# Kernel optimization log

Measured on AMD Instinct MI355X. Metric: run time of the kernel, lower is better.

Reference implementation:

```python
import jax, jax.numpy as jnp
import numpy as np

FULL_ROW, FULL_COL = 512, 1024   # input_size
ROW, COL = 64, 128               # input_size / ratio 8
N_SAMPLE = ROW * COL             # 8192 sampled pixels
NUM_CLASSES = 19
C = 512                          # feature dim hardcoded in source


def setup_inputs() -> dict:
    key = jax.random.key(0)
    k1, k2, k3 = jax.random.split(key, 3)
    features_tensor = jax.random.normal(k1, (1, C, FULL_ROW, FULL_COL), jnp.float32)
    outputs = jax.random.normal(k2, (1, NUM_CLASSES, FULL_ROW, FULL_COL), jnp.float32)
    classes_prototypes = jax.random.normal(k3, (1, NUM_CLASSES, C), jnp.float32)
    # random.sample -> unique sorted indices into the full h*w grid
    idx = np.sort(np.random.default_rng(0).choice(FULL_ROW * FULL_COL, N_SAMPLE, replace=False))
    sample_index = jnp.asarray(idx, dtype=jnp.int32)
    return {
        "features_tensor": features_tensor,
        "outputs": outputs,
        "classes_prototypes": classes_prototypes,
        "sample_index": sample_index,
    }


def reference(features_tensor, outputs, classes_prototypes, sample_index):
    hw = FULL_ROW * FULL_COL
    # gather sampled pixel features: (1,C,H,W) -> (H*W, C) -> (N_SAMPLE, C)
    feats = features_tensor.transpose(0, 2, 3, 1).reshape(hw, C)[sample_index]
    # predicted class per sampled pixel (softmax over classes preserves argmax)
    class_ids = jnp.argmax(outputs[0], axis=0).reshape(hw)[sample_index]  # (N_SAMPLE,)
    protos = classes_prototypes[0]  # (NUM_CLASSES, C)
    # squared euclidean distance, clamped (disparity_mode 'E', dim==3 path)
    d = (jnp.sum(feats * feats, axis=-1, keepdims=True)
         - 2.0 * feats @ protos.T
         + jnp.sum(protos * protos, axis=-1))            # (N_SAMPLE, NUM_CLASSES)
    d = jnp.clip(d, 1e-12, None)
    # ascending sort -> rank of the predicted class among prototype distances
    order = jnp.argsort(d, axis=1)                        # (N_SAMPLE, NUM_CLASSES)
    rank = jnp.argmax(order == class_ids[:, None], axis=1)
    score = rank.astype(jnp.float32) / float(NUM_CLASSES - 1)
    # scatter scores back into the full-resolution map
    full = jnp.zeros(hw, jnp.float32).at[sample_index].set(score)
    return full.reshape(FULL_ROW, FULL_COL)
```

## Files before the change

kernel.cpp:

```cpp
#include <hip/hip_runtime.h>
#include <hip/hip_bf16.h>
#include <math.h>

#define FSE_HW   524288
#define FSE_C    512
#define FSE_K    19
#define FSE_NS   8192
#define FSE_GS   16
#define FSE_NBLK (FSE_NS / FSE_GS)

__device__ __forceinline__ int pIdx(int c, int k) { return c * FSE_K + k + (c >> 5); }

__global__ __launch_bounds__(256) void fse_zero_kernel(float4* __restrict__ out) {
    int i = blockIdx.x * 256 + threadIdx.x;
    out[i] = make_float4(0.f, 0.f, 0.f, 0.f);
}

__global__ __launch_bounds__(256) void fse_main_kernel(
        const float* __restrict__ feats,
        const float* __restrict__ outs,
        const float* __restrict__ protos,
        const int*   __restrict__ sidx,
        float* __restrict__ out)
{
    __shared__ float  sP[FSE_C * FSE_K + 16];
    __shared__ float  sLog[FSE_GS * FSE_K];
    __shared__ int    sIdx[FSE_GS];
    __shared__ double sRed[4][FSE_GS * 20];

    const int tid = threadIdx.x;
    const int g   = blockIdx.x;

    if (tid < FSE_GS) sIdx[tid] = sidx[g * FSE_GS + tid];

    for (int i = tid; i < FSE_K * FSE_C; i += 256) {
        const int k = i / FSE_C, c = i % FSE_C;
        sP[pIdx(c, k)] = protos[i];
    }
    __syncthreads();

    for (int i = tid; i < FSE_GS * FSE_K; i += 256) {
        const int s = i / FSE_K, k = i % FSE_K;
        sLog[i] = outs[k * FSE_HW + sIdx[s]];
    }

    const int wave = tid >> 6, lane = tid & 63;
    const int s    = lane & 15;
    const int q    = lane >> 4;
    const int c0   = wave * 128 + q * 32;
    const float* A = feats + (size_t)c0 * FSE_HW + sIdx[s];

    double t[FSE_K];
    #pragma unroll
    for (int k = 0; k < FSE_K; ++k) t[k] = 0.0;
    double f2 = 0.0;

    #pragma unroll
    for (int j8 = 0; j8 < 4; ++j8) {
        float f[8];
        #pragma unroll
        for (int u = 0; u < 8; ++u)
            f[u] = A[(size_t)(j8 * 8 + u) * FSE_HW];
        #pragma unroll
        for (int u = 0; u < 8; ++u) {
            const int c = c0 + j8 * 8 + u;
            const double fd  = (double)f[u];
            f2 = fma(fd, fd, f2);
            const double m2f = -2.0 * fd;
            #pragma unroll
            for (int k = 0; k < FSE_K; ++k) {
                const double p = (double)sP[pIdx(c, k)];
                t[k] = fma(p, p + m2f, t[k]);
            }
        }
    }

    #pragma unroll
    for (int k = 0; k < FSE_K; ++k) {
        t[k] += __shfl_xor(t[k], 16);
        t[k] += __shfl_xor(t[k], 32);
    }
    f2 += __shfl_xor(f2, 16);
    f2 += __shfl_xor(f2, 32);

    if (lane < FSE_GS) {
        #pragma unroll
        for (int k = 0; k < FSE_K; ++k) sRed[wave][s * 20 + k] = t[k];
        sRed[wave][s * 20 + 19] = f2;
    }
    __syncthreads();

    for (int cell = tid; cell < FSE_GS * 20; cell += 256)
        sRed[0][cell] = (sRed[0][cell] + sRed[1][cell]) + (sRed[2][cell] + sRed[3][cell]);
    __syncthreads();

    if (tid < FSE_GS) {
        const int ss = tid;
        float best = sLog[ss * FSE_K];
        int   ocls = 0;
        #pragma unroll
        for (int k = 1; k < FSE_K; ++k) {
            const float v = sLog[ss * FSE_K + k];
            if (v > best) { best = v; ocls = k; }
        }
        const double f2s = sRed[0][ss * 20 + 19];
        double dc = 0.0;
        #pragma unroll
        for (int k = 0; k < FSE_K; ++k) {
            double dk = fmax(f2s + sRed[0][ss * 20 + k], 1e-12);
            if (k == ocls) dc = dk;
        }
        int rank = 0;
        #pragma unroll
        for (int k = 0; k < FSE_K; ++k) {
            double dk = fmax(f2s + sRed[0][ss * 20 + k], 1e-12);
            rank += (int)((dk < dc) || (dk == dc && k < ocls));
        }
        out[sIdx[ss]] = (float)rank * (1.0f / 18.0f);
    }
}

extern "C" void kernel_launch(void* const* d_in, const int* in_sizes, int n_in,
                              void* d_out, int out_size, void* d_ws, size_t ws_size,
                              hipStream_t stream) {
    const float* feats  = (const float*)d_in[0];
    const float* outs   = (const float*)d_in[1];
    const float* protos = (const float*)d_in[2];
    const int*   sidx   = (const int*)d_in[3];
    float* out = (float*)d_out;

    fse_zero_kernel<<<FSE_HW / 4 / 256, 256, 0, stream>>>((float4*)out);
    fse_main_kernel<<<FSE_NBLK, 256, 0, stream>>>(feats, outs, protos, sidx, out);
}
```

Before: 99.69 us.

## Split channel reduction across blocks with workspace partials and finalize kernel

Splits the 512-channel distance accumulation into 4 channel blocks, so the grid grows from 512 to 2048 blocks. Each block loads only its 128-channel slice of the prototypes and writes double-precision partial sums to workspace. A separate finalize kernel sums the partials, does the argmax over logits and computes the rank. This targets low occupancy and the long serial gather latency per thread, at the cost of an extra launch and a workspace round trip. The old fused kernel remains as a fallback when the workspace is too small.

```diff
diff --git a/kernel.cpp b/kernel.cpp
--- a/kernel.cpp
+++ b/kernel.cpp
@@ -6,21 +6,131 @@
 #define FSE_C    512
 #define FSE_K    19
 #define FSE_NS   8192
+#define FSE_CB   128
+#define FSE_NCB  4
 #define FSE_GS   16
-#define FSE_NBLK (FSE_NS / FSE_GS)
-
-__device__ __forceinline__ int pIdx(int c, int k) { return c * FSE_K + k + (c >> 5); }
+#define FSE_SG   (FSE_NS / FSE_GS)
 
 __global__ __launch_bounds__(256) void fse_zero_kernel(float4* __restrict__ out) {
     int i = blockIdx.x * 256 + threadIdx.x;
     out[i] = make_float4(0.f, 0.f, 0.f, 0.f);
 }
 
-__global__ __launch_bounds__(256) void fse_main_kernel(
+__global__ __launch_bounds__(256, 6) void fse_partial_kernel(
         const float* __restrict__ feats,
-        const float* __restrict__ outs,
         const float* __restrict__ protos,
         const int*   __restrict__ sidx,
+        double*      __restrict__ ws)
+{
+    __shared__ float  sPp[FSE_CB * FSE_K];
+    __shared__ int    sIdx[FSE_GS];
+    __shared__ double sRed[4][FSE_GS][20];
+
+    const int tid  = threadIdx.x;
+    const int cblk = blockIdx.x >> 9;
+    const int sg   = blockIdx.x & 511;
+
+    if (tid < FSE_GS) sIdx[tid] = sidx[sg * FSE_GS + tid];
+
+    for (int i = tid; i < FSE_CB * FSE_K; i += 256) {
+        const int k = i >> 7, cl = i & (FSE_CB - 1);
+        sPp[cl * FSE_K + k] = protos[k * FSE_C + cblk * FSE_CB + cl];
+    }
+    __syncthreads();
+
+    const int wave = tid >> 6, lane = tid & 63;
+    const int s   = lane & 15;
+    const int q   = lane >> 4;
+    const int cl0 = wave * 32 + q * 8;
+    const float* A = feats + (size_t)(cblk * FSE_CB + cl0) * FSE_HW + sIdx[s];
+
+    float f[8];
+    #pragma unroll
+    for (int u = 0; u < 8; ++u) f[u] = A[(size_t)u * FSE_HW];
+
+    double t[FSE_K];
+    #pragma unroll
+    for (int k = 0; k < FSE_K; ++k) t[k] = 0.0;
+    double f2 = 0.0;
+
+    #pragma unroll
+    for (int u = 0; u < 8; ++u) {
+        const int cl = cl0 + u;
+        const double fd  = (double)f[u];
+        f2 = fma(fd, fd, f2);
+        const double m2f = -2.0 * fd;
+        #pragma unroll
+        for (int k = 0; k < FSE_K; ++k) {
+            const double p = (double)sPp[cl * FSE_K + k];
+            t[k] = fma(p, p + m2f, t[k]);
+        }
+    }
+
+    #pragma unroll
+    for (int k = 0; k < FSE_K; ++k) {
+        t[k] += __shfl_xor(t[k], 16);
+        t[k] += __shfl_xor(t[k], 32);
+    }
+    f2 += __shfl_xor(f2, 16);
+    f2 += __shfl_xor(f2, 32);
+
+    if (lane < FSE_GS) {
+        #pragma unroll
+        for (int k = 0; k < FSE_K; ++k) sRed[wave][s][k] = t[k];
+        sRed[wave][s][19] = f2;
+    }
+    __syncthreads();
+
+    for (int cell = tid; cell < FSE_GS * 20; cell += 256) {
+        const int ss = cell / 20, j = cell % 20;
+        const double v = (sRed[0][ss][j] + sRed[1][ss][j])
+                       + (sRed[2][ss][j] + sRed[3][ss][j]);
+        ws[(size_t)(sg * FSE_GS + ss) * (FSE_NCB * 20) + cblk * 20 + j] = v;
+    }
+}
+
+__global__ __launch_bounds__(128) void fse_finalize_kernel(
+        const float*  __restrict__ outs,
+        const int*    __restrict__ sidx,
+        const double* __restrict__ ws,
+        float*        __restrict__ out)
+{
+    const int sId = blockIdx.x * 128 + threadIdx.x;
+    const int idx = sidx[sId];
+
+    float best = outs[idx];
+    int   ocls = 0;
+    #pragma unroll
+    for (int k = 1; k < FSE_K; ++k) {
+        const float v = outs[(size_t)k * FSE_HW + idx];
+        if (v > best) { best = v; ocls = k; }
+    }
+
+    const double* W = ws + (size_t)sId * (FSE_NCB * 20);
+    double t[20];
+    #pragma unroll
+    for (int j = 0; j < 20; ++j)
+        t[j] = (W[j] + W[20 + j]) + (W[40 + j] + W[60 + j]);
+
+    const double f2 = t[19];
+    double dc = 0.0;
+    #pragma unroll
+    for (int k = 0; k < FSE_K; ++k) {
+        double dk = fmax(f2 + t[k], 1e-12);
+        if (k == ocls) dc = dk;
+    }
+    int rank = 0;
+    #pragma unroll
+    for (int k = 0; k < FSE_K; ++k) {
+        double dk = fmax(f2 + t[k], 1e-12);
+        rank += (int)((dk < dc) || (dk == dc && k < ocls));
+    }
+    out[idx] = (float)rank * (1.0f / 18.0f);
+}
+
+__global__ __launch_bounds__(256) void fse_main_kernel(
+        const float* __restrict__ feats, const float* __restrict__ outs,
+        const float* __restrict__ protos, const int* __restrict__ sidx,
         float* __restrict__ out)
 {
     __shared__ float  sP[FSE_C * FSE_K + 16];
@@ -30,74 +140,58 @@
 
     const int tid = threadIdx.x;
     const int g   = blockIdx.x;
-
     if (tid < FSE_GS) sIdx[tid] = sidx[g * FSE_GS + tid];
-
     for (int i = tid; i < FSE_K * FSE_C; i += 256) {
         const int k = i / FSE_C, c = i % FSE_C;
-        sP[pIdx(c, k)] = protos[i];
-    }
-    __syncthreads();
-
+        sP[c * FSE_K + k + (c >> 5)] = protos[i];
+    }
+    __syncthreads();
     for (int i = tid; i < FSE_GS * FSE_K; i += 256) {
         const int s = i / FSE_K, k = i % FSE_K;
         sLog[i] = outs[k * FSE_HW + sIdx[s]];
     }
-
     const int wave = tid >> 6, lane = tid & 63;
-    const int s    = lane & 15;
-    const int q    = lane >> 4;
-    const int c0   = wave * 128 + q * 32;
+    const int s = lane & 15, q = lane >> 4;
+    const int c0 = wave * 128 + q * 32;
     const float* A = feats + (size_t)c0 * FSE_HW + sIdx[s];
-
     double t[FSE_K];
     #pragma unroll
     for (int k = 0; k < FSE_K; ++k) t[k] = 0.0;
     double f2 = 0.0;
-
     #pragma unroll
     for (int j8 = 0; j8 < 4; ++j8) {
         float f[8];
         #pragma unroll
-        for (int u = 0; u < 8; ++u)
-            f[u] = A[(size_t)(j8 * 8 + u) * FSE_HW];
+        for (int u = 0; u < 8; ++u) f[u] = A[(size_t)(j8 * 8 + u) * FSE_HW];
         #pragma unroll
         for (int u = 0; u < 8; ++u) {
             const int c = c0 + j8 * 8 + u;
-            const double fd  = (double)f[u];
+            const double fd = (double)f[u];
             f2 = fma(fd, fd, f2);
             const double m2f = -2.0 * fd;
             #pragma unroll
             for (int k = 0; k < FSE_K; ++k) {
-                const double p = (double)sP[pIdx(c, k)];
+                const double p = (double)sP[c * FSE_K + k + (c >> 5)];
                 t[k] = fma(p, p + m2f, t[k]);
             }
         }
     }
-
-    #pragma unroll
-    for (int k = 0; k < FSE_K; ++k) {
-        t[k] += __shfl_xor(t[k], 16);
-        t[k] += __shfl_xor(t[k], 32);
-    }
-    f2 += __shfl_xor(f2, 16);
-    f2 += __shfl_xor(f2, 32);
-
+    #pragma unroll
+    for (int k = 0; k < FSE_K; ++k) { t[k] += __shfl_xor(t[k], 16); t[k] += __shfl_xor(t[k], 32); }
+    f2 += __shfl_xor(f2, 16); f2 += __shfl_xor(f2, 32);
     if (lane < FSE_GS) {
         #pragma unroll
         for (int k = 0; k < FSE_K; ++k) sRed[wave][s * 20 + k] = t[k];
         sRed[wave][s * 20 + 19] = f2;
     }
     __syncthreads();
-
     for (int cell = tid; cell < FSE_GS * 20; cell += 256)
         sRed[0][cell] = (sRed[0][cell] + sRed[1][cell]) + (sRed[2][cell] + sRed[3][cell]);
     __syncthreads();
-
     if (tid < FSE_GS) {
         const int ss = tid;
         float best = sLog[ss * FSE_K];
-        int   ocls = 0;
+        int ocls = 0;
         #pragma unroll
         for (int k = 1; k < FSE_K; ++k) {
             const float v = sLog[ss * FSE_K + k];
@@ -130,5 +224,14 @@
     float* out = (float*)d_out;
 
     fse_zero_kernel<<<FSE_HW / 4 / 256, 256, 0, stream>>>((float4*)out);
-    fse_main_kernel<<<FSE_NBLK, 256, 0, stream>>>(feats, outs, protos, sidx, out);
-}
+
+    const size_t ws_need = (size_t)FSE_NS * FSE_NCB * 20 * sizeof(double);
+    if (ws_size >= ws_need) {
+        fse_partial_kernel<<<FSE_NCB * FSE_SG, 256, 0, stream>>>(
+            feats, protos, sidx, (double*)d_ws);
+        fse_finalize_kernel<<<FSE_NS / 128, 128, 0, stream>>>(
+            outs, sidx, (const double*)d_ws, out);
+    } else {
+        fse_main_kernel<<<FSE_SG, 256, 0, stream>>>(feats, outs, protos, sidx, out);
+    }
+}
```

New measurement: 118.0 us. 18.3% more time.
